# Optimization experiments

Measured on AMD Instinct MI355X. Metric: run time of the kernel, lower is better.

The kernel has to match this reference:

```python
import jax, jax.numpy as jnp
import numpy as np

THETA_BASE = 10000.0


def _rope_tables(head_dim, seq_len):
    # intended math of precompute_rope_params (source has an arange typo;
    # standard RoPE: inv_freq over even indices)
    inv_freq = 1.0 / (THETA_BASE ** (jnp.arange(0, head_dim, 2, dtype=jnp.float32) / head_dim))
    pos = jnp.arange(seq_len, dtype=jnp.float32)
    angles = pos[:, None] * inv_freq[None, :]          # [S, hd/2]
    angles = jnp.concatenate([angles, angles], axis=1)  # [S, hd]
    return jnp.cos(angles), jnp.sin(angles)


def _apply_rope(x, cos, sin):
    # x: [B, H, S, hd]; cos/sin: [S, hd] broadcast over batch/heads
    hd = x.shape[-1]
    x1, x2 = x[..., : hd // 2], x[..., hd // 2 :]
    rotated = jnp.concatenate([-x2, x1], axis=-1)
    return x * cos + rotated * sin


def setup_inputs() -> dict:
    key = jax.random.key(0)
    ks = jax.random.split(key, 5)
    b, s, d = 2, 2048, 1024
    x = jax.random.normal(ks[0], (b, s, d), dtype=jnp.float32)
    # store weights as [d_in, d_out] so y = x @ W (equivalent math to nn.Linear)
    scale = 1.0 / np.sqrt(d)
    W_q = jax.random.normal(ks[1], (d, d), dtype=jnp.float32) * scale
    W_k = jax.random.normal(ks[2], (d, d), dtype=jnp.float32) * scale
    W_v = jax.random.normal(ks[3], (d, d), dtype=jnp.float32) * scale
    W_o = jax.random.normal(ks[4], (d, d), dtype=jnp.float32) * scale
    return {"x": x, "W_q": W_q, "W_k": W_k, "W_v": W_v, "W_o": W_o}


def reference(x, W_q, W_k, W_v, W_o):
    num_heads = 16
    b, s, d_in = x.shape
    d_out = W_q.shape[1]
    hd = d_out // num_heads

    def split_heads(t):  # [B,S,D] -> [B,H,S,hd]
        return t.reshape(b, s, num_heads, hd).transpose(0, 2, 1, 3)

    q = split_heads(x @ W_q)
    k = split_heads(x @ W_k)
    v = split_heads(x @ W_v)

    cos, sin = _rope_tables(hd, s)
    q = _apply_rope(q, cos, sin)
    k = _apply_rope(k, cos, sin)

    scores = jnp.einsum("bhqd,bhkd->bhqk", q, k)
    causal = jnp.triu(jnp.ones((s, s), dtype=bool), k=1)  # True above diagonal
    scores = jnp.where(causal, -jnp.inf, scores)
    attn = jax.nn.softmax(scores / jnp.sqrt(jnp.float32(hd)), axis=-1)

    ctx = jnp.einsum("bhqk,bhkd->bhqd", attn, v)
    ctx = ctx.transpose(0, 2, 1, 3).reshape(b, s, d_out)
    return ctx @ W_o
```

## Files before the change

kernel.cpp:

```cpp
#include <hip/hip_runtime.h>

typedef __bf16 bf16x8 __attribute__((ext_vector_type(8)));
typedef float f32x4 __attribute__((ext_vector_type(4)));
typedef unsigned short u16;

__device__ __forceinline__ u16 f2bf(float f){
  union { float fp; unsigned int u; } v; v.fp = f;
  unsigned int r = v.u + 0x7fffu + ((v.u >> 16) & 1u);
  return (u16)(r >> 16);
}

__device__ __forceinline__ void glds16(const void* g, void* l){
  __builtin_amdgcn_global_load_lds((__attribute__((address_space(1))) void*)(void*)(g),
                                   (__attribute__((address_space(3))) void*)(l), 16, 0, 0);
}

__global__ __launch_bounds__(256) void convert_x_k(const float* __restrict__ in, u16* __restrict__ out, int n4){
  int stride = gridDim.x * blockDim.x;
  for (int i = blockIdx.x*blockDim.x + threadIdx.x; i < n4; i += stride){
    float4 v = ((const float4*)in)[i];
    ushort4 o;
    o.x = f2bf(v.x); o.y = f2bf(v.y); o.z = f2bf(v.z); o.w = f2bf(v.w);
    ((ushort4*)out)[i] = o;
  }
}

__global__ __launch_bounds__(256) void transpose_w_k(const float* __restrict__ W0, const float* __restrict__ W1,
                                                     const float* __restrict__ W2, const float* __restrict__ W3,
                                                     u16* __restrict__ Wt){
  __shared__ float tile[32][33];
  const float* W = (blockIdx.z==0)?W0:(blockIdx.z==1)?W1:(blockIdx.z==2)?W2:W3;
  u16* dst = Wt + ((size_t)blockIdx.z<<20);
  int tx = threadIdx.x, ty = threadIdx.y;
  int x = blockIdx.x*32 + tx;
  int y0 = blockIdx.y*32;
  #pragma unroll
  for (int i=0;i<32;i+=8) tile[ty+i][tx] = W[(size_t)(y0+ty+i)*1024 + x];
  __syncthreads();
  int xo = y0 + tx;
  #pragma unroll
  for (int i=0;i<32;i+=8) dst[(size_t)(blockIdx.x*32+ty+i)*1024 + xo] = f2bf(tile[tx][ty+i]);
}

__global__ __launch_bounds__(256) void rope_tables_k(float* __restrict__ cosT, float* __restrict__ sinT){
  int i = blockIdx.x*256 + threadIdx.x;
  int si = i>>6, dd = i&63, f = dd&31;
  float invf = exp2f(-13.287712379549449f * (float)f * (1.0f/32.0f));
  float ang = (float)si * invf;
  float s, c;
  sincosf(ang, &s, &c);
  cosT[i] = c; sinT[i] = s;
}

__global__ __launch_bounds__(256,3) void gemm_qkv_k(const u16* __restrict__ xb, const u16* __restrict__ Wt,
                                                  const float* __restrict__ cosT, const float* __restrict__ sinT,
                                                  u16* __restrict__ Qr, u16* __restrict__ Kr, u16* __restrict__ Vt){
  __shared__ __align__(16) u16 As[128*32];
  __shared__ __align__(16) u16 Bs[128*32];
  const int tid = threadIdx.x;
  const int w = tid>>6, lane = tid&63, quad = lane>>4, l15 = lane&15;
  const int wrow = w>>1, wcol = w&1;
  const int m0 = blockIdx.x*128;
  const int nG0 = blockIdx.y*128;
  const int which = nG0>>10, n0 = nG0&1023;
  const u16* __restrict__ B = Wt + ((size_t)which<<20);
  f32x4 acc[4][4] = {};
  const int srow = lane>>2, scol = (lane&3)*8;
  const int ar0 = m0 + 32*w + srow;
  const int br0 = n0 + 32*w + srow;

  for (int kb=0; kb<1024; kb+=32){
    glds16(&xb[(size_t)ar0*1024      + kb + scol], &As[(32*w)*32]);
    glds16(&xb[(size_t)(ar0+16)*1024 + kb + scol], &As[(32*w+16)*32]);
    glds16(&B [(size_t)br0*1024      + kb + scol], &Bs[(32*w)*32]);
    glds16(&B [(size_t)(br0+16)*1024 + kb + scol], &Bs[(32*w+16)*32]);
    __syncthreads();
    bf16x8 a[4], b[4];
    #pragma unroll
    for (int t=0;t<4;t++){
      a[t] = *(const bf16x8*)&As[(64*wrow + 16*t + l15)*32 + quad*8];
      b[t] = *(const bf16x8*)&Bs[(64*wcol + 16*t + l15)*32 + quad*8];
    }
    #pragma unroll
    for (int ti=0;ti<4;ti++)
      #pragma unroll
      for (int tj=0;tj<4;tj++)
        acc[ti][tj] = __builtin_amdgcn_mfma_f32_16x16x32_bf16(a[ti], b[tj], acc[ti][tj], 0,0,0);
    __syncthreads();
  }

  const int colbase = n0 + 64*wcol;
  const int hh = colbase>>6;
  const int rowbase = m0 + 64*wrow + 4*quad;
  const float QSCALE = 0.18033688011112042f;

  if (which < 2){
    u16* __restrict__ out = (which==0) ? Qr : Kr;
    const float osc = (which==0) ? QSCALE : 1.0f;
    #pragma unroll
    for (int tj=0;tj<4;tj++){
      int dd = 16*tj + l15;
      int obase = (dd>>5)*512 + ((dd>>3)&3)*128 + (dd&7);
      float sgn = (tj<2) ? -1.0f : 1.0f;
      int pj = tj^2;
      #pragma unroll
      for (int ti=0;ti<4;ti++){
        #pragma unroll
        for (int r=0;r<4;r++){
          int m = rowbase + 16*ti + r;
          int bi = m>>11, si = m&2047;
          float cs = cosT[(si<<6)+dd];
          float sn = sinT[(si<<6)+dd];
          float vv = (acc[ti][tj][r]*cs + sgn*acc[ti][pj][r]*sn) * osc;
          out[((size_t)(bi*16+hh)<<17) + (si>>4)*1024 + (si&15)*8 + obase] = f2bf(vv);
        }
      }
    }
  } else {
    #pragma unroll
    for (int tj=0;tj<4;tj++){
      #pragma unroll
      for (int ti=0;ti<4;ti++){
        int m = rowbase + 16*ti;
        int bi = m>>11, si = m&2047;
        ushort4 pk;
        pk.x = f2bf(acc[ti][tj][0]); pk.y = f2bf(acc[ti][tj][1]);
        pk.z = f2bf(acc[ti][tj][2]); pk.w = f2bf(acc[ti][tj][3]);
        *(ushort4*)&Vt[((size_t)(bi*16+hh)<<17) + (si>>6)*4096 + ((si>>5)&1)*2048
                       + tj*512 + ((si>>3)&3)*128 + l15*8 + (si&7)] = pk;
      }
    }
  }
}

__global__ __launch_bounds__(256,3) void attn_k(const u16* __restrict__ QF, const u16* __restrict__ KF,
                                                const u16* __restrict__ VF, u16* __restrict__ ctx){
  __shared__ __align__(16) u16 SC[4*4608];
  __shared__ float LL[4][32];
  const int tid = threadIdx.x;
  const int w = tid>>6, lane = tid&63, quad = lane>>4, l15 = lane&15;
  const int uu = w>>1, kpar = w&1;
  const int Lin = blockIdx.x + (gridDim.x * blockIdx.y);
  const int xcd = Lin & 7, slot = Lin >> 3;
  const int bh = (xcd<<2) | (slot>>4);
  const int p = 2*(slot & 15) + uu;
  const u16* __restrict__ Qb = QF + ((size_t)bh<<17);
  const u16* __restrict__ Kb = KF + ((size_t)bh<<17);
  const u16* __restrict__ Vb = VF + ((size_t)bh<<17);
  u16* __restrict__ Pw = SC + w*4608;
  const int loff = lane*8;
  const int bi = bh>>4, hh = bh&15;

  #pragma unroll 1
  for (int ph=0; ph<2; ph++){
    if (ph) __syncthreads();
    const int tile = ph ? (63-p) : p;
    const int q0 = tile*32;
    const int nk = (tile>>1) + 1;

    bf16x8 qf[2][2];
    #pragma unroll
    for (int ti=0;ti<2;ti++)
      #pragma unroll
      for (int kh=0;kh<2;kh++)
        qf[ti][kh] = *(const bf16x8*)&Qb[(2*tile+ti)*1024 + kh*512 + loff];

    f32x4 o[2][4] = {};
    float ls[2] = {0.f, 0.f};

    for (int kt = kpar; kt < nk; kt += 2){
      const int k0 = kt*64;
      bf16x8 kf[4][2], vf[4][2];
      #pragma unroll
      for (int tjk=0;tjk<4;tjk++)
        #pragma unroll
        for (int kh=0;kh<2;kh++)
          kf[tjk][kh] = *(const bf16x8*)&Kb[(4*kt+tjk)*1024 + kh*512 + loff];
      #pragma unroll
      for (int tjd=0;tjd<4;tjd++)
        #pragma unroll
        for (int kh=0;kh<2;kh++)
          vf[tjd][kh] = *(const bf16x8*)&Vb[kt*4096 + kh*2048 + tjd*512 + loff];

      f32x4 st[2][4] = {};
      #pragma unroll
      for (int ti=0;ti<2;ti++)
        #pragma unroll
        for (int tjk=0;tjk<4;tjk++){
          st[ti][tjk] = __builtin_amdgcn_mfma_f32_16x16x32_bf16(kf[tjk][0], qf[ti][0], st[ti][tjk], 0,0,0);
          st[ti][tjk] = __builtin_amdgcn_mfma_f32_16x16x32_bf16(kf[tjk][1], qf[ti][1], st[ti][tjk], 0,0,0);
        }

      #pragma unroll
      for (int ti=0;ti<2;ti++){
        const int qbase = q0 + 16*ti;
        f32x4 pv[4];
        if (k0 + 63 > qbase){
          const int qg = qbase + l15;
          #pragma unroll
          for (int tjk=0;tjk<4;tjk++)
            #pragma unroll
            for (int r=0;r<4;r++){
              int kg = k0 + 16*tjk + 4*quad + r;
              pv[tjk][r] = (kg > qg) ? 0.0f : exp2f(fminf(st[ti][tjk][r], 80.0f));
            }
        } else {
          #pragma unroll
          for (int tjk=0;tjk<4;tjk++)
            #pragma unroll
            for (int r=0;r<4;r++)
              pv[tjk][r] = exp2f(fminf(st[ti][tjk][r], 80.0f));
        }
        f32x4 t4 = (pv[0]+pv[1]) + (pv[2]+pv[3]);
        float rs = (t4[0]+t4[1]) + (t4[2]+t4[3]);
        rs += __shfl_xor(rs, 16, 64);
        rs += __shfl_xor(rs, 32, 64);
        ls[ti] += rs;
        #pragma unroll
        for (int tjk=0;tjk<4;tjk++){
          ushort4 pk;
          pk.x = f2bf(pv[tjk][0]); pk.y = f2bf(pv[tjk][1]);
          pk.z = f2bf(pv[tjk][2]); pk.w = f2bf(pv[tjk][3]);
          *(ushort4*)&Pw[(16*ti + l15)*72 + 16*tjk + 4*quad] = pk;
        }
      }

      bf16x8 pf[2][2];
      #pragma unroll
      for (int ti=0;ti<2;ti++)
        #pragma unroll
        for (int kh=0;kh<2;kh++)
          pf[ti][kh] = *(const bf16x8*)&Pw[(16*ti + l15)*72 + 32*kh + quad*8];
      #pragma unroll
      for (int ti=0;ti<2;ti++)
        #pragma unroll
        for (int tjd=0;tjd<4;tjd++){
          o[ti][tjd] = __builtin_amdgcn_mfma_f32_16x16x32_bf16(pf[ti][0], vf[tjd][0], o[ti][tjd], 0,0,0);
          o[ti][tjd] = __builtin_amdgcn_mfma_f32_16x16x32_bf16(pf[ti][1], vf[tjd][1], o[ti][tjd], 0,0,0);
        }
    }

    float* __restrict__ Ob = (float*)&SC[w*4608];
    #pragma unroll
    for (int ti=0;ti<2;ti++)
      #pragma unroll
      for (int tjd=0;tjd<4;tjd++)
        *(f32x4*)&Ob[(16*tjd + l15)*36 + 16*ti + 4*quad] = o[ti][tjd];
    if (quad == 0){
      LL[w][l15]      = ls[0];
      LL[w][16 + l15] = ls[1];
    }
    __syncthreads();

    if (kpar == ph){
      const int pw = uu*2 + (kpar^1);
      const float* __restrict__ Op = (const float*)&SC[pw*4608];
      const float* __restrict__ Lp = LL[pw];
      #pragma unroll
      for (int ti=0;ti<2;ti++){
        f32x4 om[4];
        #pragma unroll
        for (int tjd=0;tjd<4;tjd++)
          om[tjd] = o[ti][tjd] + *(const f32x4*)&Op[(16*tjd + l15)*36 + 16*ti + 4*quad];
        #pragma unroll
        for (int r=0;r<4;r++){
          float lv = Lp[16*ti + 4*quad + r] + __shfl(ls[ti], 4*quad + r, 64);
          float inv = 1.0f / lv;
          int sq = q0 + 16*ti + 4*quad + r;
          u16* orow = ctx + (((size_t)(bi*2048 + sq))<<10) + (hh<<6);
          #pragma unroll
          for (int tjd=0;tjd<4;tjd++)
            orow[16*tjd + l15] = f2bf(om[tjd][r] * inv);
        }
      }
    }
  }
}

__global__ __launch_bounds__(256,3) void gemm_out_k(const u16* __restrict__ cb, const u16* __restrict__ Wot,
                                                  float* __restrict__ out){
  __shared__ __align__(16) u16 As[128*32];
  __shared__ __align__(16) u16 Bs[128*32];
  const int tid = threadIdx.x;
  const int w = tid>>6, lane = tid&63, quad = lane>>4, l15 = lane&15;
  const int wrow = w>>1, wcol = w&1;
  const int m0 = blockIdx.x*128;
  const int nG0 = blockIdx.y*128;
  f32x4 acc[4][4] = {};
  const int srow = lane>>2, scol = (lane&3)*8;
  const int ar0 = m0 + 32*w + srow;
  const int br0 = nG0 + 32*w + srow;

  for (int kb=0; kb<1024; kb+=32){
    glds16(&cb [(size_t)ar0*1024      + kb + scol], &As[(32*w)*32]);
    glds16(&cb [(size_t)(ar0+16)*1024 + kb + scol], &As[(32*w+16)*32]);
    glds16(&Wot[(size_t)br0*1024      + kb + scol], &Bs[(32*w)*32]);
    glds16(&Wot[(size_t)(br0+16)*1024 + kb + scol], &Bs[(32*w+16)*32]);
    __syncthreads();
    bf16x8 a[4], b[4];
    #pragma unroll
    for (int t=0;t<4;t++){
      a[t] = *(const bf16x8*)&As[(64*wrow + 16*t + l15)*32 + quad*8];
      b[t] = *(const bf16x8*)&Bs[(64*wcol + 16*t + l15)*32 + quad*8];
    }
    #pragma unroll
    for (int ti=0;ti<4;ti++)
      #pragma unroll
      for (int tj=0;tj<4;tj++)
        acc[ti][tj] = __builtin_amdgcn_mfma_f32_16x16x32_bf16(a[ti], b[tj], acc[ti][tj], 0,0,0);
    __syncthreads();
  }

  const int rowbase = m0 + 64*wrow + 4*quad;
  const int colb = nG0 + 64*wcol;
  #pragma unroll
  for (int ti=0;ti<4;ti++){
    #pragma unroll
    for (int r=0;r<4;r++){
      int m = rowbase + 16*ti + r;
      float* orow = out + (size_t)m*1024 + colb;
      #pragma unroll
      for (int tj=0;tj<4;tj++)
        orow[16*tj + l15] = acc[ti][tj][r];
    }
  }
}

extern "C" void kernel_launch(void* const* d_in, const int* in_sizes, int n_in,
                              void* d_out, int out_size, void* d_ws, size_t ws_size,
                              hipStream_t stream){
  const float* x  = (const float*)d_in[0];
  const float* Wq = (const float*)d_in[1];
  const float* Wk = (const float*)d_in[2];
  const float* Wv = (const float*)d_in[3];
  const float* Wo = (const float*)d_in[4];
  float* out = (float*)d_out;
  u16* ws = (u16*)d_ws;

  u16* XB  = ws;
  u16* WT  = ws + ((size_t)4<<20);
  u16* QFp = ws + ((size_t)8<<20);
  u16* KFp = ws + ((size_t)12<<20);
  u16* VFp = ws + ((size_t)16<<20);
  u16* CTX = ws + ((size_t)20<<20);
  float* COS = (float*)(ws + ((size_t)24<<20));
  float* SIN = COS + (1<<17);

  convert_x_k  <<<512, 256, 0, stream>>>(x, XB, 1<<20);
  transpose_w_k<<<dim3(32,32,4), dim3(32,8), 0, stream>>>(Wq, Wk, Wv, Wo, WT);
  rope_tables_k<<<512, 256, 0, stream>>>(COS, SIN);
  gemm_qkv_k   <<<dim3(32,24), 256, 0, stream>>>(XB, WT, COS, SIN, QFp, KFp, VFp);
  attn_k       <<<dim3(16,32), 256, 0, stream>>>(QFp, KFp, VFp, CTX);
  gemm_out_k   <<<dim3(32,8), 256, 0, stream>>>(CTX, WT + ((size_t)3<<20), out);
}
```

Before: 194.1 us.

## Fuse prep kernels and split attention KV loop across four waves per tile

Merges the x conversion, weight transpose and RoPE table kernels into a single prep launch, removing two kernel launches. The attention kernel now gives each block a single 32-row query tile per phase and spreads its KV blocks over all four waves rather than two. Partial outputs and row sums from all four waves are then reduced through shared memory, and each wave writes one 16-column slice. P is packed to bf16 with a byte-permute truncation instead of round-to-nearest, which is cheaper but adds a small precision bias. Short causal tiles leave some waves idle, and the four-way reduction adds LDS traffic.

```diff
diff --git a/kernel.cpp b/kernel.cpp
--- a/kernel.cpp
+++ b/kernel.cpp
@@ -10,46 +10,53 @@
   return (u16)(r >> 16);
 }
 
+__device__ __forceinline__ unsigned pk2(float a, float b){
+  union { float f; unsigned u; } ua, ub; ua.f = a; ub.f = b;
+  return __builtin_amdgcn_perm(ub.u, ua.u, 0x07060302u);
+}
+
 __device__ __forceinline__ void glds16(const void* g, void* l){
   __builtin_amdgcn_global_load_lds((__attribute__((address_space(1))) void*)(void*)(g),
                                    (__attribute__((address_space(3))) void*)(l), 16, 0, 0);
 }
 
-__global__ __launch_bounds__(256) void convert_x_k(const float* __restrict__ in, u16* __restrict__ out, int n4){
-  int stride = gridDim.x * blockDim.x;
-  for (int i = blockIdx.x*blockDim.x + threadIdx.x; i < n4; i += stride){
-    float4 v = ((const float4*)in)[i];
-    ushort4 o;
-    o.x = f2bf(v.x); o.y = f2bf(v.y); o.z = f2bf(v.z); o.w = f2bf(v.w);
-    ((ushort4*)out)[i] = o;
-  }
-}
-
-__global__ __launch_bounds__(256) void transpose_w_k(const float* __restrict__ W0, const float* __restrict__ W1,
-                                                     const float* __restrict__ W2, const float* __restrict__ W3,
-                                                     u16* __restrict__ Wt){
-  __shared__ float tile[32][33];
-  const float* W = (blockIdx.z==0)?W0:(blockIdx.z==1)?W1:(blockIdx.z==2)?W2:W3;
-  u16* dst = Wt + ((size_t)blockIdx.z<<20);
-  int tx = threadIdx.x, ty = threadIdx.y;
-  int x = blockIdx.x*32 + tx;
-  int y0 = blockIdx.y*32;
-  #pragma unroll
-  for (int i=0;i<32;i+=8) tile[ty+i][tx] = W[(size_t)(y0+ty+i)*1024 + x];
-  __syncthreads();
-  int xo = y0 + tx;
-  #pragma unroll
-  for (int i=0;i<32;i+=8) dst[(size_t)(blockIdx.x*32+ty+i)*1024 + xo] = f2bf(tile[tx][ty+i]);
-}
-
-__global__ __launch_bounds__(256) void rope_tables_k(float* __restrict__ cosT, float* __restrict__ sinT){
-  int i = blockIdx.x*256 + threadIdx.x;
-  int si = i>>6, dd = i&63, f = dd&31;
-  float invf = exp2f(-13.287712379549449f * (float)f * (1.0f/32.0f));
-  float ang = (float)si * invf;
-  float s, c;
-  sincosf(ang, &s, &c);
-  cosT[i] = c; sinT[i] = s;
+__global__ __launch_bounds__(256) void prep_k(const float* __restrict__ x,
+                                              const float* __restrict__ W0, const float* __restrict__ W1,
+                                              const float* __restrict__ W2, const float* __restrict__ W3,
+                                              u16* __restrict__ XB, u16* __restrict__ Wt,
+                                              float* __restrict__ cosT, float* __restrict__ sinT){
+  const int b = blockIdx.x, tid = threadIdx.x;
+  if (b < 512){
+    for (int i = b*256 + tid; i < (1<<20); i += 512*256){
+      float4 v = ((const float4*)x)[i];
+      ushort4 o;
+      o.x = f2bf(v.x); o.y = f2bf(v.y); o.z = f2bf(v.z); o.w = f2bf(v.w);
+      ((ushort4*)XB)[i] = o;
+    }
+  } else if (b < 4608){
+    __shared__ float tile[32][33];
+    const int b2 = b - 512;
+    const int bz = b2>>10, by = (b2>>5)&31, bx = b2&31;
+    const float* W = (bz==0)?W0:(bz==1)?W1:(bz==2)?W2:W3;
+    u16* dst = Wt + ((size_t)bz<<20);
+    const int tx = tid&31, ty = tid>>5;
+    const int xx = bx*32 + tx;
+    const int y0 = by*32;
+    #pragma unroll
+    for (int i=0;i<32;i+=8) tile[ty+i][tx] = W[(size_t)(y0+ty+i)*1024 + xx];
+    __syncthreads();
+    const int xo = y0 + tx;
+    #pragma unroll
+    for (int i=0;i<32;i+=8) dst[(size_t)(bx*32+ty+i)*1024 + xo] = f2bf(tile[tx][ty+i]);
+  } else {
+    const int i = (b-4608)*256 + tid;
+    const int si = i>>6, dd = i&63, f = dd&31;
+    float invf = exp2f(-13.287712379549449f * (float)f * (1.0f/32.0f));
+    float ang = (float)si * invf;
+    float s, c;
+    sincosf(ang, &s, &c);
+    cosT[i] = c; sinT[i] = s;
+  }
 }
 
 __global__ __launch_bounds__(256,3) void gemm_qkv_k(const u16* __restrict__ xb, const u16* __restrict__ Wt,
@@ -139,11 +146,10 @@
   __shared__ float LL[4][32];
   const int tid = threadIdx.x;
   const int w = tid>>6, lane = tid&63, quad = lane>>4, l15 = lane&15;
-  const int uu = w>>1, kpar = w&1;
-  const int Lin = blockIdx.x + (gridDim.x * blockIdx.y);
+  const int Lin = blockIdx.x;
   const int xcd = Lin & 7, slot = Lin >> 3;
-  const int bh = (xcd<<2) | (slot>>4);
-  const int p = 2*(slot & 15) + uu;
+  const int bh = (xcd<<2) | (slot>>5);
+  const int p = slot & 31;
   const u16* __restrict__ Qb = QF + ((size_t)bh<<17);
   const u16* __restrict__ Kb = KF + ((size_t)bh<<17);
   const u16* __restrict__ Vb = VF + ((size_t)bh<<17);
@@ -168,7 +174,7 @@
     f32x4 o[2][4] = {};
     float ls[2] = {0.f, 0.f};
 
-    for (int kt = kpar; kt < nk; kt += 2){
+    for (int kt = w; kt < nk; kt += 4){
       const int k0 = kt*64;
       bf16x8 kf[4][2], vf[4][2];
       #pragma unroll
@@ -218,10 +224,10 @@
         ls[ti] += rs;
         #pragma unroll
         for (int tjk=0;tjk<4;tjk++){
-          ushort4 pk;
-          pk.x = f2bf(pv[tjk][0]); pk.y = f2bf(pv[tjk][1]);
-          pk.z = f2bf(pv[tjk][2]); pk.w = f2bf(pv[tjk][3]);
-          *(ushort4*)&Pw[(16*ti + l15)*72 + 16*tjk + 4*quad] = pk;
+          uint2 pk;
+          pk.x = pk2(pv[tjk][0], pv[tjk][1]);
+          pk.y = pk2(pv[tjk][2], pv[tjk][3]);
+          *(uint2*)&Pw[(16*ti + l15)*72 + 16*tjk + 4*quad] = pk;
         }
       }
 
@@ -252,26 +258,18 @@
     }
     __syncthreads();
 
-    if (kpar == ph){
-      const int pw = uu*2 + (kpar^1);
-      const float* __restrict__ Op = (const float*)&SC[pw*4608];
-      const float* __restrict__ Lp = LL[pw];
-      #pragma unroll
-      for (int ti=0;ti<2;ti++){
-        f32x4 om[4];
-        #pragma unroll
-        for (int tjd=0;tjd<4;tjd++)
-          om[tjd] = o[ti][tjd] + *(const f32x4*)&Op[(16*tjd + l15)*36 + 16*ti + 4*quad];
-        #pragma unroll
-        for (int r=0;r<4;r++){
-          float lv = Lp[16*ti + 4*quad + r] + __shfl(ls[ti], 4*quad + r, 64);
-          float inv = 1.0f / lv;
-          int sq = q0 + 16*ti + 4*quad + r;
-          u16* orow = ctx + (((size_t)(bi*2048 + sq))<<10) + (hh<<6);
-          #pragma unroll
-          for (int tjd=0;tjd<4;tjd++)
-            orow[16*tjd + l15] = f2bf(om[tjd][r] * inv);
-        }
+    #pragma unroll
+    for (int ti=0;ti<2;ti++){
+      f32x4 om = {0.f,0.f,0.f,0.f};
+      #pragma unroll
+      for (int w2=0;w2<4;w2++)
+        om += *(const f32x4*)&((const float*)&SC[w2*4608])[(16*w + l15)*36 + 16*ti + 4*quad];
+      #pragma unroll
+      for (int r=0;r<4;r++){
+        int ridx = 16*ti + 4*quad + r;
+        float lv = LL[0][ridx] + LL[1][ridx] + LL[2][ridx] + LL[3][ridx];
+        int sq = q0 + ridx;
+        ctx[(((size_t)(bi*2048 + sq))<<10) + (hh<<6) + 16*w + l15] = f2bf(om[r] / lv);
       }
     }
   }
@@ -346,10 +344,8 @@
   float* COS = (float*)(ws + ((size_t)24<<20));
   float* SIN = COS + (1<<17);
 
-  convert_x_k  <<<512, 256, 0, stream>>>(x, XB, 1<<20);
-  transpose_w_k<<<dim3(32,32,4), dim3(32,8), 0, stream>>>(Wq, Wk, Wv, Wo, WT);
-  rope_tables_k<<<512, 256, 0, stream>>>(COS, SIN);
+  prep_k       <<<5120, 256, 0, stream>>>(x, Wq, Wk, Wv, Wo, XB, WT, COS, SIN);
   gemm_qkv_k   <<<dim3(32,24), 256, 0, stream>>>(XB, WT, COS, SIN, QFp, KFp, VFp);
-  attn_k       <<<dim3(16,32), 256, 0, stream>>>(QFp, KFp, VFp, CTX);
+  attn_k       <<<1024, 256, 0, stream>>>(QFp, KFp, VFp, CTX);
   gemm_out_k   <<<dim3(32,8), 256, 0, stream>>>(CTX, WT + ((size_t)3<<20), out);
 }
```

After: 184.5 us. 5.0% less time.
